# Performance work log

Measured on AMD Instinct MI355X. Metric: run time of the kernel, lower is better.

The kernel has to match this reference:

```python
import jax, jax.numpy as jnp
import numpy as np

B, S, D, H, HD, MLP = 2, 4096, 512, 8, 64, 2048
BLK, C = 128, 32  # Fixed1Pattern(block_size=128), Fixed2Pattern(block_size=128, c=32)
EPS = 1e-6


def _xavier(key, shape, fan_in, fan_out):
    lim = np.sqrt(6.0 / (fan_in + fan_out)).astype(np.float32)
    return jax.random.uniform(key, shape, jnp.float32, -lim, lim)


def setup_inputs() -> dict:
    key = jax.random.key(0)
    ks = jax.random.split(key, 9)
    return {
        "inputs": jax.random.normal(ks[0], (B, S, D), jnp.float32),
        "ln1_scale": jnp.ones((D,), jnp.float32),
        "ln1_bias": jnp.zeros((D,), jnp.float32),
        "wq": _xavier(ks[1], (D, H, HD), D, H * HD),
        "wk": _xavier(ks[2], (D, H, HD), D, H * HD),
        "wv": _xavier(ks[3], (D, H, HD), D, H * HD),
        "wo": _xavier(ks[4], (H, HD, D), H * HD, D),
        "ln2_scale": jnp.ones((D,), jnp.float32),
        "ln2_bias": jnp.zeros((D,), jnp.float32),
        "w1": _xavier(ks[5], (D, MLP), D, MLP),
        "b1": jax.random.normal(ks[6], (MLP,), jnp.float32) * 1e-6,
        "w2": _xavier(ks[7], (MLP, D), MLP, D),
        "b2": jax.random.normal(ks[8], (D,), jnp.float32) * 1e-6,
    }


def _layer_norm(x, scale, bias):
    mu = jnp.mean(x, axis=-1, keepdims=True)
    var = jnp.mean(jnp.square(x - mu), axis=-1, keepdims=True)
    return (x - mu) * jax.lax.rsqrt(var + EPS) * scale + bias


def _sparse_mask():
    # Union of causal Fixed1 (same block) and Fixed2 (last C columns of each block) patterns.
    i = jnp.arange(S)[:, None]
    j = jnp.arange(S)[None, :]
    causal = j <= i
    local = (i // BLK) == (j // BLK)            # Fixed1: within-block
    strided = (j % BLK) >= (BLK - C)            # Fixed2: block-summary columns
    return causal & (local | strided)           # [S, S] bool


def reference(inputs, ln1_scale, ln1_bias, wq, wk, wv, wo,
              ln2_scale, ln2_bias, w1, b1, w2, b2):
    x = _layer_norm(inputs, ln1_scale, ln1_bias)
    q = jnp.einsum("bsd,dhk->bshk", x, wq)
    k = jnp.einsum("bsd,dhk->bshk", x, wk)
    v = jnp.einsum("bsd,dhk->bshk", x, wv)
    scale = 1.0 / np.sqrt(HD).astype(np.float32)
    scores = jnp.einsum("bqhk,bshk->bhqs", q * scale, k)  # [B,H,S,S]
    mask = _sparse_mask()[None, None]
    scores = jnp.where(mask, scores, jnp.float32(-1e9))
    attn = jax.nn.softmax(scores, axis=-1)
    ctx = jnp.einsum("bhqs,bshk->bqhk", attn, v)
    attn_out = jnp.einsum("bqhk,hkd->bqd", ctx, wo)
    x = attn_out + inputs  # residual 1 (dropout deterministic)
    y = _layer_norm(x, ln2_scale, ln2_bias)
    y = jax.nn.gelu(y @ w1 + b1) @ w2 + b2  # MlpBlock
    return x + y
```

## Files before the change

kernel.cpp:

```cpp
#include <hip/hip_runtime.h>
#include <hip/hip_bf16.h>

typedef __attribute__((ext_vector_type(8))) __bf16 bf16x8;
typedef __attribute__((ext_vector_type(8))) short s16x8;
typedef __attribute__((ext_vector_type(4))) float f32x4;

#define NB 2
#define NS 4096
#define ND 512
#define NH 8
#define NHD 64
#define NMLP 2048

__device__ __forceinline__ unsigned short f2b(float f) {
  __hip_bfloat16 h = __float2bfloat16(f);
  return __builtin_bit_cast(unsigned short, h);
}

__device__ __forceinline__ float b2f(unsigned short u) {
  unsigned int x = (unsigned int)u << 16;
  return __builtin_bit_cast(float, x);
}

__device__ __forceinline__ float geluf(float x) {
  float u = 0.7978845608028654f * (x + 0.044715f * x * x * x);
  return x / (1.0f + __expf(-2.0f * u));
}

__device__ __forceinline__ float exp2_fast(float x) {
  float r;
  asm("v_exp_f32 %0, %1" : "=v"(r) : "v"(x));
  return r;
}

__device__ __forceinline__ void gload16(const void* g, void* l) {
  __builtin_amdgcn_global_load_lds((const __attribute__((address_space(1))) void*)g,
                                   (__attribute__((address_space(3))) void*)l, 16, 0, 0);
}

__global__ __launch_bounds__(256) void prep_ln(const float* __restrict__ wq,
                                               const float* __restrict__ wk,
                                               const float* __restrict__ wv,
                                               const float* __restrict__ wo,
                                               const float* __restrict__ w1,
                                               const float* __restrict__ w2,
                                               unsigned short* __restrict__ qkvT,
                                               unsigned short* __restrict__ woT,
                                               unsigned short* __restrict__ w1T,
                                               unsigned short* __restrict__ w2T,
                                               const float* __restrict__ x,
                                               const float* __restrict__ g,
                                               const float* __restrict__ bta,
                                               unsigned short* __restrict__ xout) {
  __shared__ unsigned short lt[64][66];
  const int t = threadIdx.x;
  if (blockIdx.x < 768) {
    const int tile = blockIdx.x;
    const float* src;
    unsigned short* dst;
    int R, C, tr, tc;
    float sc = 1.0f;
    if (tile < 256) {
      int seg = tile >> 6, tt = tile & 63;
      R = 512; C = 512;
      src = seg == 0 ? wq : seg == 1 ? wk : seg == 2 ? wv : wo;
      dst = (seg < 3) ? (qkvT + ((size_t)seg << 18)) : woT;
      if (seg == 0) sc = 0.18033688011112042f;
      tr = tt >> 3; tc = tt & 7;
    } else if (tile < 512) {
      int tt = tile - 256;
      R = 512; C = 2048; src = w1; dst = w1T;
      tr = tt >> 5; tc = tt & 31;
    } else {
      int tt = tile - 512;
      R = 2048; C = 512; src = w2; dst = w2T;
      tr = tt >> 3; tc = tt & 7;
    }
    const int r0 = tr * 64, c0 = tc * 64;
    const int fx = t & 15, fy = t >> 4;
#pragma unroll
    for (int p = 0; p < 4; ++p) {
      int rr = p * 16 + fy;
      float4 v = *(const float4*)&src[(size_t)(r0 + rr) * C + c0 + fx * 4];
      lt[rr][fx * 4 + 0] = f2b(v.x * sc);
      lt[rr][fx * 4 + 1] = f2b(v.y * sc);
      lt[rr][fx * 4 + 2] = f2b(v.z * sc);
      lt[rr][fx * 4 + 3] = f2b(v.w * sc);
    }
    __syncthreads();
#pragma unroll
    for (int p = 0; p < 4; ++p) {
      int cc = p * 16 + fy;
      ushort4 o;
      o.x = lt[fx * 4 + 0][cc];
      o.y = lt[fx * 4 + 1][cc];
      o.z = lt[fx * 4 + 2][cc];
      o.w = lt[fx * 4 + 3][cc];
      *(ushort4*)&dst[(size_t)(c0 + cc) * R + r0 + fx * 4] = o;
    }
  } else {
    const int l = t & 63, w = t >> 6;
    const size_t row = (size_t)(blockIdx.x - 768) * 4 + w;
    const float4* xr = (const float4*)(x + row * ND);
    float4 a = xr[l];
    float4 bq = xr[64 + l];
    float s = a.x + a.y + a.z + a.w + bq.x + bq.y + bq.z + bq.w;
    float ss = a.x * a.x + a.y * a.y + a.z * a.z + a.w * a.w +
               bq.x * bq.x + bq.y * bq.y + bq.z * bq.z + bq.w * bq.w;
#pragma unroll
    for (int msk = 1; msk <= 32; msk <<= 1) {
      s += __shfl_xor(s, msk);
      ss += __shfl_xor(ss, msk);
    }
    float mu = s * (1.0f / ND);
    float var = ss * (1.0f / ND) - mu * mu;
    float rr = rsqrtf(var + 1e-6f);
    const float4* g4 = (const float4*)g;
    const float4* b4 = (const float4*)bta;
    float4 g0 = g4[l], g1 = g4[64 + l], b0 = b4[l], b1 = b4[64 + l];
    ushort4 o0, o1;
    o0.x = f2b((a.x - mu) * rr * g0.x + b0.x);
    o0.y = f2b((a.y - mu) * rr * g0.y + b0.y);
    o0.z = f2b((a.z - mu) * rr * g0.z + b0.z);
    o0.w = f2b((a.w - mu) * rr * g0.w + b0.w);
    o1.x = f2b((bq.x - mu) * rr * g1.x + b1.x);
    o1.y = f2b((bq.y - mu) * rr * g1.y + b1.y);
    o1.z = f2b((bq.z - mu) * rr * g1.z + b1.z);
    o1.w = f2b((bq.w - mu) * rr * g1.w + b1.w);
    ushort4* orow = (ushort4*)(xout + row * ND);
    orow[l] = o0;
    orow[64 + l] = o1;
  }
}

__global__ __launch_bounds__(256) void ln_bf16_in(const unsigned short* __restrict__ x,
                                                  const float* __restrict__ g,
                                                  const float* __restrict__ bta,
                                                  unsigned short* __restrict__ out) {
  const int t = threadIdx.x, l = t & 63, w = t >> 6;
  const size_t row = (size_t)blockIdx.x * 4 + w;
  const s16x8 v = *(const s16x8*)&x[row * ND + l * 8];
  float xv[8];
  float s = 0.0f, ss = 0.0f;
#pragma unroll
  for (int i = 0; i < 8; ++i) {
    xv[i] = b2f((unsigned short)v[i]);
    s += xv[i];
    ss += xv[i] * xv[i];
  }
#pragma unroll
  for (int msk = 1; msk <= 32; msk <<= 1) {
    s += __shfl_xor(s, msk);
    ss += __shfl_xor(ss, msk);
  }
  float mu = s * (1.0f / ND);
  float var = ss * (1.0f / ND) - mu * mu;
  float rr = rsqrtf(var + 1e-6f);
  const float4* g4 = (const float4*)g;
  const float4* b4 = (const float4*)bta;
  float4 g0 = g4[2 * l], g1 = g4[2 * l + 1];
  float4 b0 = b4[2 * l], b1 = b4[2 * l + 1];
  s16x8 o;
  o[0] = (short)f2b((xv[0] - mu) * rr * g0.x + b0.x);
  o[1] = (short)f2b((xv[1] - mu) * rr * g0.y + b0.y);
  o[2] = (short)f2b((xv[2] - mu) * rr * g0.z + b0.z);
  o[3] = (short)f2b((xv[3] - mu) * rr * g0.w + b0.w);
  o[4] = (short)f2b((xv[4] - mu) * rr * g1.x + b1.x);
  o[5] = (short)f2b((xv[5] - mu) * rr * g1.y + b1.y);
  o[6] = (short)f2b((xv[6] - mu) * rr * g1.z + b1.z);
  o[7] = (short)f2b((xv[7] - mu) * rr * g1.w + b1.w);
  *(s16x8*)&out[row * ND + l * 8] = o;
}

template <int EPI>
__global__ __launch_bounds__(512) void gemm_bt(const unsigned short* __restrict__ A,
                                               const unsigned short* __restrict__ Bt,
                                               int M, int N, int K,
                                               unsigned short* __restrict__ ob,
                                               float* __restrict__ of,
                                               const float* __restrict__ addf,
                                               const float* __restrict__ bias) {
  __shared__ unsigned short lA[2][128 * 64];
  __shared__ unsigned short lB[2][128 * 64];
  const int t = threadIdx.x;
  const int l = t & 63, w = t >> 6;
  const int wr = w >> 2, wc = w & 3;
  const int gx = gridDim.x;
  const int nwg = gx * gridDim.y;
  const int fid = blockIdx.y * gx + blockIdx.x;
  const int q8 = nwg >> 3, r8 = nwg & 7, xcd = fid & 7, idx = fid >> 3;
  const int lid = (xcd < r8 ? xcd * (q8 + 1) : r8 * (q8 + 1) + (xcd - r8) * q8) + idx;
  const int bm = lid / gx, bn = lid % gx;
  const size_t rowBytes = (size_t)K * 2;
  const char* Ab = (const char*)A + (size_t)bm * 128 * rowBytes;
  const char* Bb = (const char*)Bt + (size_t)bn * 128 * rowBytes;
  const int sr0 = t >> 3;
  const int scb = (((t & 7) ^ ((t >> 3) & 7)) << 4);
  f32x4 acc[4][2] = {};

  auto stage = [&](int buf, int k0) {
    char* dA = (char*)&lA[buf][0] + t * 16;
    char* dB = (char*)&lB[buf][0] + t * 16;
#pragma unroll
    for (int i = 0; i < 2; ++i) {
      const size_t go = (size_t)(sr0 + i * 64) * rowBytes + 2 * k0 + scb;
      gload16(Ab + go, dA + i * 8192);
      gload16(Bb + go, dB + i * 8192);
    }
  };

  const int nkt = K >> 6;
  stage(0, 0);
  int cur = 0;
  for (int kt = 0; kt < nkt; ++kt) {
    if (kt + 1 < nkt) {
      stage(cur ^ 1, (kt + 1) * 64);
      asm volatile("s_waitcnt vmcnt(4)" ::: "memory");
    } else {
      asm volatile("s_waitcnt vmcnt(0)" ::: "memory");
    }
    __builtin_amdgcn_s_barrier();
    __builtin_amdgcn_sched_barrier(0);
#pragma unroll
    for (int ks = 0; ks < 2; ++ks) {
      const int xg = ((ks * 4 + (l >> 4)) ^ (l & 7)) * 8;
      bf16x8 aF[4], bF[2];
#pragma unroll
      for (int m = 0; m < 4; ++m)
        aF[m] = *(const bf16x8*)&lA[cur][(wr * 64 + m * 16 + (l & 15)) * 64 + xg];
#pragma unroll
      for (int n = 0; n < 2; ++n)
        bF[n] = *(const bf16x8*)&lB[cur][(wc * 32 + n * 16 + (l & 15)) * 64 + xg];
      __builtin_amdgcn_s_setprio(1);
#pragma unroll
      for (int m = 0; m < 4; ++m)
#pragma unroll
        for (int n = 0; n < 2; ++n)
          acc[m][n] = __builtin_amdgcn_mfma_f32_16x16x32_bf16(aF[m], bF[n], acc[m][n], 0, 0, 0);
      __builtin_amdgcn_s_setprio(0);
    }
    asm volatile("s_waitcnt lgkmcnt(0)" ::: "memory");
    __builtin_amdgcn_s_barrier();
    cur ^= 1;
  }
#pragma unroll
  for (int m = 0; m < 4; ++m)
#pragma unroll
    for (int n = 0; n < 2; ++n) {
      int row0 = bm * 128 + wr * 64 + m * 16 + (l >> 4) * 4;
      int col = bn * 128 + wc * 32 + n * 16 + (l & 15);
      if constexpr (EPI == 2) {
#pragma unroll
        for (int j = 0; j < 4; ++j) {
          size_t i = (size_t)(row0 + j) * NMLP + col;
          ob[i] = f2b(geluf(acc[m][n][j] + bias[col]));
        }
      } else {
#pragma unroll
        for (int j = 0; j < 4; ++j) {
          size_t i = (size_t)(row0 + j) * ND + col;
          of[i] = acc[m][n][j] + addf[i];
        }
      }
    }
}

template <int EPI>
__global__ __launch_bounds__(256) void gemm_bt64(const unsigned short* __restrict__ A,
                                                 const unsigned short* __restrict__ Bt,
                                                 int M, int N, int K,
                                                 unsigned short* __restrict__ ob,
                                                 float* __restrict__ of,
                                                 const float* __restrict__ addf,
                                                 const float* __restrict__ bias,
                                                 const unsigned short* __restrict__ addb) {
  __shared__ unsigned short lA[2][128 * 64];
  __shared__ unsigned short lB[2][64 * 64];
  const int t = threadIdx.x;
  const int l = t & 63, w = t >> 6;
  const int wr = w >> 1, wc = w & 1;
  const int gx = gridDim.x;
  const int nwg = gx * gridDim.y;
  const int fid = blockIdx.y * gx + blockIdx.x;
  const int q8 = nwg >> 3, r8 = nwg & 7, xcd = fid & 7, idx = fid >> 3;
  const int lid = (xcd < r8 ? xcd * (q8 + 1) : r8 * (q8 + 1) + (xcd - r8) * q8) + idx;
  const int bm = lid / gx, bn = lid % gx;
  const size_t rowBytes = (size_t)K * 2;
  const char* Ab = (const char*)A + (size_t)bm * 128 * rowBytes;
  const char* Bb = (const char*)Bt + (size_t)bn * 64 * rowBytes;
  const int sr0 = t >> 3;
  const int scb = (((t & 7) ^ ((t >> 3) & 7)) << 4);
  f32x4 acc[4][2] = {};

  auto stage = [&](int buf, int k0) {
    char* dA = (char*)&lA[buf][0] + t * 16;
#pragma unroll
    for (int i = 0; i < 4; ++i) {
      const size_t go = (size_t)(sr0 + i * 32) * rowBytes + 2 * k0 + scb;
      gload16(Ab + go, dA + i * 4096);
    }
    char* dB = (char*)&lB[buf][0] + t * 16;
#pragma unroll
    for (int i = 0; i < 2; ++i) {
      const size_t go = (size_t)(sr0 + i * 32) * rowBytes + 2 * k0 + scb;
      gload16(Bb + go, dB + i * 4096);
    }
  };

  const int nkt = K >> 6;
  stage(0, 0);
  int cur = 0;
  for (int kt = 0; kt < nkt; ++kt) {
    if (kt + 1 < nkt) {
      stage(cur ^ 1, (kt + 1) * 64);
      asm volatile("s_waitcnt vmcnt(6)" ::: "memory");
    } else {
      asm volatile("s_waitcnt vmcnt(0)" ::: "memory");
    }
    __builtin_amdgcn_s_barrier();
    __builtin_amdgcn_sched_barrier(0);
#pragma unroll
    for (int ks = 0; ks < 2; ++ks) {
      const int xg = ((ks * 4 + (l >> 4)) ^ (l & 7)) * 8;
      bf16x8 aF[4], bF[2];
#pragma unroll
      for (int m = 0; m < 4; ++m)
        aF[m] = *(const bf16x8*)&lA[cur][(wr * 64 + m * 16 + (l & 15)) * 64 + xg];
#pragma unroll
      for (int n = 0; n < 2; ++n)
        bF[n] = *(const bf16x8*)&lB[cur][(wc * 32 + n * 16 + (l & 15)) * 64 + xg];
      __builtin_amdgcn_s_setprio(1);
#pragma unroll
      for (int m = 0; m < 4; ++m)
#pragma unroll
        for (int n = 0; n < 2; ++n)
          acc[m][n] = __builtin_amdgcn_mfma_f32_16x16x32_bf16(aF[m], bF[n], acc[m][n], 0, 0, 0);
      __builtin_amdgcn_s_setprio(0);
    }
    asm volatile("s_waitcnt lgkmcnt(0)" ::: "memory");
    __builtin_amdgcn_s_barrier();
    cur ^= 1;
  }
#pragma unroll
  for (int m = 0; m < 4; ++m)
#pragma unroll
    for (int n = 0; n < 2; ++n) {
      int row0 = bm * 128 + wr * 64 + m * 16 + (l >> 4) * 4;
      int col = bn * 64 + wc * 32 + n * 16 + (l & 15);
      if constexpr (EPI == 0) {
        int part = col >> 9, nn = col & 511;
        int hh = nn >> 6, hd = nn & 63;
        int b = row0 >> 12, sidx0 = row0 & 4095;
        if (part < 2) {
#pragma unroll
          for (int j = 0; j < 4; ++j)
            ob[((((size_t)part * NB + b) * NH + hh) * NS + sidx0 + j) * NHD + hd] =
                f2b(acc[m][n][j]);
        } else {
          ushort4 o;
          o.x = f2b(acc[m][n][0]);
          o.y = f2b(acc[m][n][1]);
          o.z = f2b(acc[m][n][2]);
          o.w = f2b(acc[m][n][3]);
          *(ushort4*)&ob[(size_t)2 * NB * NH * NS * NHD +
                         (((size_t)b * NH + hh) * NHD + hd) * NS + sidx0] = o;
        }
      } else if constexpr (EPI == 1) {
#pragma unroll
        for (int j = 0; j < 4; ++j) {
          size_t i = (size_t)(row0 + j) * ND + col;
          ob[i] = f2b(acc[m][n][j] + addf[i]);
        }
      } else {
#pragma unroll
        for (int j = 0; j < 4; ++j) {
          size_t i = (size_t)(row0 + j) * ND + col;
          of[i] = acc[m][n][j] + bias[col] + b2f(addb[i]);
        }
      }
    }
}

__global__ __launch_bounds__(512, 4) void attn_sparse(const unsigned short* __restrict__ qm,
                                                      const unsigned short* __restrict__ km,
                                                      const unsigned short* __restrict__ vTg,
                                                      unsigned short* __restrict__ ctx) {
  __shared__ unsigned short kl[2][128 * 64];
  __shared__ unsigned short vt[2][64 * 128];
  __shared__ unsigned short pl[8][16 * 64];
  const int t = threadIdx.x, l = t & 63, w = t >> 6;
  const int bid = blockIdx.x;
  const int hh = bid & 7;
  const int jj = bid >> 3;
  const int b = jj >> 5;
  const int qb = (jj < 32) ? jj : 63 - jj;
  const size_t bh = ((size_t)b * NH + hh) * NS;
  const size_t bhd = ((size_t)b * NH + hh) * NHD;
  const int qrow0 = qb * 128 + w * 16;
  bf16x8 qa[2];
#pragma unroll
  for (int ks = 0; ks < 2; ++ks)
    qa[ks] = *(const bf16x8*)&qm[(bh + qrow0 + (l & 15)) * NHD + ks * 32 + (l >> 4) * 8];
  f32x4 c[4] = {};
  float mrun[4], lrun[4];
#pragma unroll
  for (int j = 0; j < 4; ++j) { mrun[j] = -1e30f; lrun[j] = 0.0f; }

  const int nsum128 = qb >> 2, rem = qb & 3;
  const int nSumCh = nsum128 + (rem ? 1 : 0);
  const int nch = nSumCh + 1;

  const int kr_ = t >> 3;
  const int ku_ = (t & 7) ^ (kr_ & 7);
  const int vr_ = t >> 4;
  const int vu_ = ((t & 15) & 8) | (((t & 15) & 7) ^ (vr_ & 7));

  auto keyOf = [&](int c2, int kk) -> int {
    return (c2 < nSumCh) ? ((c2 * 4 + (kk >> 5)) * 128 + 96 + (kk & 31)) : (qb * 128 + kk);
  };
  auto stage = [&](int buf, int c2) {
    const int krow0 = keyOf(c2, kr_);
    gload16(&km[(bh + krow0) * NHD + ku_ * 8], (char*)&kl[buf][0] + t * 16);
    const int krow1 = keyOf(c2, kr_ + 64);
    gload16(&km[(bh + krow1) * NHD + ku_ * 8], (char*)&kl[buf][0] + 8192 + t * 16);
    const int gk = keyOf(c2, vu_ * 8);
    gload16(&vTg[(bhd + vr_) * NS + gk], (char*)&vt[buf][0] + t * 16);
    gload16(&vTg[(bhd + vr_ + 32) * NS + gk], (char*)&vt[buf][0] + 8192 + t * 16);
  };

  const int e_ = l & 7, q_ = l >> 4;
  const int kx0 = (q_ ^ e_) * 8;
  const int kx1 = ((4 + q_) ^ e_) * 8;
  const int r4_ = (q_ & 1) << 2;

  stage(0, 0);
  int cur = 0;
  for (int ch = 0; ch < nch; ++ch) {
    if (ch + 1 < nch) {
      stage(cur ^ 1, ch + 1);
      asm volatile("s_waitcnt vmcnt(4)" ::: "memory");
    } else {
      asm volatile("s_waitcnt vmcnt(0)" ::: "memory");
    }
    __builtin_amdgcn_s_barrier();
    __builtin_amdgcn_sched_barrier(0);

    const bool isLocal = (ch == nch - 1);
    const bool isRem = (rem != 0) && !isLocal && (ch == nsum128);
    const int nT = isLocal ? (w + 1) : (isRem ? 2 * rem : 8);
    const int nTpl = isLocal ? ((w | 1) + 1) : nT;
    const int nKs = nTpl >> 1;

    f32x4 sf[8];
#pragma unroll
    for (int n = 0; n < 8; ++n) {
      if (n < nT) {
        const int row = n * 16 + (l & 15);
        const bf16x8 k0 = *(const bf16x8*)&kl[cur][row * 64 + kx0];
        const bf16x8 k1 = *(const bf16x8*)&kl[cur][row * 64 + kx1];
        f32x4 a = {};
        a = __builtin_amdgcn_mfma_f32_16x16x32_bf16(qa[0], k0, a, 0, 0, 0);
        a = __builtin_amdgcn_mfma_f32_16x16x32_bf16(qa[1], k1, a, 0, 0, 0);
        if (isLocal && n == w) {
#pragma unroll
          for (int j = 0; j < 4; ++j)
            if ((l & 15) > q_ * 4 + j) a[j] = -1e9f;
        }
        sf[n] = a;
      }
    }
    float cm[4];
#pragma unroll
    for (int j = 0; j < 4; ++j) cm[j] = -1e30f;
#pragma unroll
    for (int n = 0; n < 8; ++n)
      if (n < nT)
#pragma unroll
        for (int j = 0; j < 4; ++j) cm[j] = fmaxf(cm[j], sf[n][j]);
#pragma unroll
    for (int j = 0; j < 4; ++j) {
      cm[j] = fmaxf(cm[j], __shfl_xor(cm[j], 1));
      cm[j] = fmaxf(cm[j], __shfl_xor(cm[j], 2));
      cm[j] = fmaxf(cm[j], __shfl_xor(cm[j], 4));
      cm[j] = fmaxf(cm[j], __shfl_xor(cm[j], 8));
    }
    bool need = false;
#pragma unroll
    for (int j = 0; j < 4; ++j) need |= (cm[j] > mrun[j] + 11.5416f);
    if (__any(need)) {
      float al[4];
#pragma unroll
      for (int j = 0; j < 4; ++j) {
        float nm = fmaxf(mrun[j], cm[j]);
        al[j] = exp2_fast(mrun[j] - nm);
        mrun[j] = nm;
      }
#pragma unroll
      for (int n = 0; n < 4; ++n)
#pragma unroll
        for (int j = 0; j < 4; ++j) c[n][j] *= al[j];
#pragma unroll
      for (int j = 0; j < 4; ++j) lrun[j] *= al[j];
    }
    float rs[4] = {0.f, 0.f, 0.f, 0.f};
#pragma unroll
    for (int n = 0; n < 8; ++n)
      if (n < nT)
#pragma unroll
        for (int j = 0; j < 4; ++j) {
          float p = exp2_fast(sf[n][j] - mrun[j]);
          sf[n][j] = p;
          rs[j] += p;
        }
#pragma unroll
    for (int j = 0; j < 4; ++j) {
      rs[j] += __shfl_xor(rs[j], 1);
      rs[j] += __shfl_xor(rs[j], 2);
      rs[j] += __shfl_xor(rs[j], 4);
      rs[j] += __shfl_xor(rs[j], 8);
      lrun[j] += rs[j];
    }
#pragma unroll
    for (int h = 0; h < 2; ++h) {
      if (h * 4 < nTpl) {
#pragma unroll
        for (int n2 = 0; n2 < 4; ++n2) {
          const int n = h * 4 + n2;
          const int cu = n2 * 2 + ((l >> 3) & 1);
#pragma unroll
          for (int j = 0; j < 4; ++j) {
            if (n < nTpl) {
              unsigned short pv = 0;
              if (n < nT) pv = f2b(sf[n][j]);
              const int rowp = q_ * 4 + j;
              pl[w][rowp * 64 + (cu ^ (r4_ | j)) * 8 + e_] = pv;
            }
          }
        }
#pragma unroll
        for (int ks2 = 0; ks2 < 2; ++ks2) {
          const int ks = h * 2 + ks2;
          if (ks < nKs) {
            const bf16x8 pa =
                *(const bf16x8*)&pl[w][(l & 15) * 64 + (ks2 ? kx1 : kx0)];
#pragma unroll
            for (int nd = 0; nd < 4; ++nd) {
              const bf16x8 vb = *(const bf16x8*)&vt[cur][(nd * 16 + (l & 15)) * 128 +
                                                         ((ks & 2) << 5) +
                                                         (ks2 ? kx1 : kx0)];
              c[nd] = __builtin_amdgcn_mfma_f32_16x16x32_bf16(pa, vb, c[nd], 0, 0, 0);
            }
          }
        }
      }
    }
    __builtin_amdgcn_s_barrier();
    cur ^= 1;
  }
  float rinv[4];
#pragma unroll
  for (int j = 0; j < 4; ++j) rinv[j] = 1.0f / lrun[j];
#pragma unroll
  for (int n = 0; n < 4; ++n)
#pragma unroll
    for (int j = 0; j < 4; ++j) {
      int srow = qrow0 + q_ * 4 + j;
      int col = n * 16 + (l & 15);
      ctx[((size_t)b * NS + srow) * ND + hh * NHD + col] = f2b(c[n][j] * rinv[j]);
    }
}

extern "C" void kernel_launch(void* const* d_in, const int* in_sizes, int n_in,
                              void* d_out, int out_size, void* d_ws, size_t ws_size,
                              hipStream_t stream) {
  (void)in_sizes; (void)n_in; (void)out_size; (void)ws_size;
  const float* inputs = (const float*)d_in[0];
  const float* ln1s = (const float*)d_in[1];
  const float* ln1b = (const float*)d_in[2];
  const float* wq = (const float*)d_in[3];
  const float* wk = (const float*)d_in[4];
  const float* wv = (const float*)d_in[5];
  const float* wo = (const float*)d_in[6];
  const float* ln2s = (const float*)d_in[7];
  const float* ln2b = (const float*)d_in[8];
  const float* w1 = (const float*)d_in[9];
  const float* b1 = (const float*)d_in[10];
  const float* w2 = (const float*)d_in[11];
  const float* b2 = (const float*)d_in[12];
  float* out = (float*)d_out;

  unsigned short* xln = (unsigned short*)d_ws;
  unsigned short* xln2 = xln + (size_t)8192 * 512;
  unsigned short* ctx = xln2 + (size_t)8192 * 512;
  unsigned short* qkv = ctx + (size_t)8192 * 512;
  unsigned short* xresb = qkv + (size_t)3 * 8192 * 512;
  unsigned short* hbuf = xresb + (size_t)8192 * 512;
  unsigned short* qkvT = hbuf + (size_t)8192 * 2048;
  unsigned short* woT = qkvT + (size_t)1536 * 512;
  unsigned short* w1T = woT + (size_t)512 * 512;
  unsigned short* w2T = w1T + (size_t)2048 * 512;

  prep_ln<<<2816, 256, 0, stream>>>(wq, wk, wv, wo, w1, w2, qkvT, woT, w1T, w2T,
                                    inputs, ln1s, ln1b, xln);
  gemm_bt64<0><<<dim3(24, 64), 256, 0, stream>>>(xln, qkvT, 8192, 1536, 512,
                                                 qkv, nullptr, nullptr, nullptr, nullptr);
  attn_sparse<<<512, 512, 0, stream>>>(qkv, qkv + (size_t)8192 * 512,
                                       qkv + (size_t)2 * 8192 * 512, ctx);
  gemm_bt64<1><<<dim3(8, 64), 256, 0, stream>>>(ctx, woT, 8192, 512, 512,
                                                xresb, nullptr, inputs, nullptr, nullptr);
  ln_bf16_in<<<2048, 256, 0, stream>>>(xresb, ln2s, ln2b, xln2);
  gemm_bt<2><<<dim3(16, 64), 512, 0, stream>>>(xln2, w1T, 8192, 2048, 512,
                                               hbuf, nullptr, nullptr, b1);
  gemm_bt64<3><<<dim3(8, 64), 256, 0, stream>>>(hbuf, w2T, 8192, 512, 2048,
                                                nullptr, out, nullptr, b2, xresb);
}
```

Measured before the change: 145.1 us.

## Split sparse attention into single-wave blocks loading K/V directly from global

Restructures the sparse attention kernel from 512-thread blocks, where eight waves share double-buffered K/V tiles in LDS, to 4096 single-wave blocks. Each wave reads K and V fragments straight from global memory into MFMA operands. This removes the LDS staging, the barriers and the async pipelining, and spreads work across more blocks for better load balance. In exchange, the eight waves of a query block each re-read the same K/V data, relying on L2 or L1 hits, and the loads are no longer overlapped with compute through explicit prefetching.

After: 184.1 us. +26.9%, slower.

```diff
diff --git a/kernel.cpp b/kernel.cpp
--- a/kernel.cpp
+++ b/kernel.cpp
@@ -381,22 +381,23 @@
     }
 }
 
-__global__ __launch_bounds__(512, 4) void attn_sparse(const unsigned short* __restrict__ qm,
-                                                      const unsigned short* __restrict__ km,
-                                                      const unsigned short* __restrict__ vTg,
-                                                      unsigned short* __restrict__ ctx) {
-  __shared__ unsigned short kl[2][128 * 64];
-  __shared__ unsigned short vt[2][64 * 128];
-  __shared__ unsigned short pl[8][16 * 64];
-  const int t = threadIdx.x, l = t & 63, w = t >> 6;
+__global__ __launch_bounds__(64) void attn_sparse(const unsigned short* __restrict__ qm,
+                                                  const unsigned short* __restrict__ km,
+                                                  const unsigned short* __restrict__ vTg,
+                                                  unsigned short* __restrict__ ctx) {
+  __shared__ unsigned short pl[16 * 64];
+  const int l = threadIdx.x;
   const int bid = blockIdx.x;
   const int hh = bid & 7;
-  const int jj = bid >> 3;
-  const int b = jj >> 5;
-  const int qb = (jj < 32) ? jj : 63 - jj;
+  const int u_ = bid >> 3;
+  const int wp = u_ & 7;
+  const int v_ = u_ >> 3;
+  const int b = v_ >> 5;
+  const int k_ = v_ & 31;
+  const int qb = b ? (31 - k_) : k_;
   const size_t bh = ((size_t)b * NH + hh) * NS;
   const size_t bhd = ((size_t)b * NH + hh) * NHD;
-  const int qrow0 = qb * 128 + w * 16;
+  const int qrow0 = qb * 128 + wp * 16;
   bf16x8 qa[2];
 #pragma unroll
   for (int ks = 0; ks < 2; ++ks)
@@ -410,22 +411,8 @@
   const int nSumCh = nsum128 + (rem ? 1 : 0);
   const int nch = nSumCh + 1;
 
-  const int kr_ = t >> 3;
-  const int ku_ = (t & 7) ^ (kr_ & 7);
-  const int vr_ = t >> 4;
-  const int vu_ = ((t & 15) & 8) | (((t & 15) & 7) ^ (vr_ & 7));
-
   auto keyOf = [&](int c2, int kk) -> int {
     return (c2 < nSumCh) ? ((c2 * 4 + (kk >> 5)) * 128 + 96 + (kk & 31)) : (qb * 128 + kk);
-  };
-  auto stage = [&](int buf, int c2) {
-    const int krow0 = keyOf(c2, kr_);
-    gload16(&km[(bh + krow0) * NHD + ku_ * 8], (char*)&kl[buf][0] + t * 16);
-    const int krow1 = keyOf(c2, kr_ + 64);
-    gload16(&km[(bh + krow1) * NHD + ku_ * 8], (char*)&kl[buf][0] + 8192 + t * 16);
-    const int gk = keyOf(c2, vu_ * 8);
-    gload16(&vTg[(bhd + vr_) * NS + gk], (char*)&vt[buf][0] + t * 16);
-    gload16(&vTg[(bhd + vr_ + 32) * NS + gk], (char*)&vt[buf][0] + 8192 + t * 16);
   };
 
   const int e_ = l & 7, q_ = l >> 4;
@@ -433,22 +420,11 @@
   const int kx1 = ((4 + q_) ^ e_) * 8;
   const int r4_ = (q_ & 1) << 2;
 
-  stage(0, 0);
-  int cur = 0;
   for (int ch = 0; ch < nch; ++ch) {
-    if (ch + 1 < nch) {
-      stage(cur ^ 1, ch + 1);
-      asm volatile("s_waitcnt vmcnt(4)" ::: "memory");
-    } else {
-      asm volatile("s_waitcnt vmcnt(0)" ::: "memory");
-    }
-    __builtin_amdgcn_s_barrier();
-    __builtin_amdgcn_sched_barrier(0);
-
     const bool isLocal = (ch == nch - 1);
     const bool isRem = (rem != 0) && !isLocal && (ch == nsum128);
-    const int nT = isLocal ? (w + 1) : (isRem ? 2 * rem : 8);
-    const int nTpl = isLocal ? ((w | 1) + 1) : nT;
+    const int nT = isLocal ? (wp + 1) : (isRem ? 2 * rem : 8);
+    const int nTpl = isLocal ? ((wp | 1) + 1) : nT;
     const int nKs = nTpl >> 1;
 
     f32x4 sf[8];
@@ -456,12 +432,13 @@
     for (int n = 0; n < 8; ++n) {
       if (n < nT) {
         const int row = n * 16 + (l & 15);
-        const bf16x8 k0 = *(const bf16x8*)&kl[cur][row * 64 + kx0];
-        const bf16x8 k1 = *(const bf16x8*)&kl[cur][row * 64 + kx1];
+        const unsigned short* kp = &km[(bh + keyOf(ch, row)) * NHD];
+        const bf16x8 k0 = *(const bf16x8*)&kp[q_ * 8];
+        const bf16x8 k1 = *(const bf16x8*)&kp[32 + q_ * 8];
         f32x4 a = {};
         a = __builtin_amdgcn_mfma_f32_16x16x32_bf16(qa[0], k0, a, 0, 0, 0);
         a = __builtin_amdgcn_mfma_f32_16x16x32_bf16(qa[1], k1, a, 0, 0, 0);
-        if (isLocal && n == w) {
+        if (isLocal && n == wp) {
 #pragma unroll
           for (int j = 0; j < 4; ++j)
             if ((l & 15) > q_ * 4 + j) a[j] = -1e9f;
@@ -533,7 +510,7 @@
               unsigned short pv = 0;
               if (n < nT) pv = f2b(sf[n][j]);
               const int rowp = q_ * 4 + j;
-              pl[w][rowp * 64 + (cu ^ (r4_ | j)) * 8 + e_] = pv;
+              pl[rowp * 64 + (cu ^ (r4_ | j)) * 8 + e_] = pv;
             }
           }
         }
@@ -542,20 +519,18 @@
           const int ks = h * 2 + ks2;
           if (ks < nKs) {
             const bf16x8 pa =
-                *(const bf16x8*)&pl[w][(l & 15) * 64 + (ks2 ? kx1 : kx0)];
+                *(const bf16x8*)&pl[(l & 15) * 64 + (ks2 ? kx1 : kx0)];
+            const int gkv = keyOf(ch, ks * 32 + q_ * 8);
 #pragma unroll
             for (int nd = 0; nd < 4; ++nd) {
-              const bf16x8 vb = *(const bf16x8*)&vt[cur][(nd * 16 + (l & 15)) * 128 +
-                                                         ((ks & 2) << 5) +
-                                                         (ks2 ? kx1 : kx0)];
+              const bf16x8 vb =
+                  *(const bf16x8*)&vTg[(bhd + nd * 16 + (l & 15)) * NS + gkv];
               c[nd] = __builtin_amdgcn_mfma_f32_16x16x32_bf16(pa, vb, c[nd], 0, 0, 0);
             }
           }
         }
       }
     }
-    __builtin_amdgcn_s_barrier();
-    cur ^= 1;
   }
   float rinv[4];
 #pragma unroll
@@ -604,7 +579,7 @@
                                     inputs, ln1s, ln1b, xln);
   gemm_bt64<0><<<dim3(24, 64), 256, 0, stream>>>(xln, qkvT, 8192, 1536, 512,
                                                  qkv, nullptr, nullptr, nullptr, nullptr);
-  attn_sparse<<<512, 512, 0, stream>>>(qkv, qkv + (size_t)8192 * 512,
+  attn_sparse<<<4096, 64, 0, stream>>>(qkv, qkv + (size_t)8192 * 512,
                                        qkv + (size_t)2 * 8192 * 512, ctx);
   gemm_bt64<1><<<dim3(8, 64), 256, 0, stream>>>(ctx, woT, 8192, 512, 512,
                                                 xresb, nullptr, inputs, nullptr, nullptr);
```

## Split sparse attention key chunks across two blocks and add a merge kernel

Applied to the files above, without the earlier changes.

Each (batch, head, query-block) attention task is now split into two halves over its key chunks, with 1024 blocks each writing an unnormalized partial output plus running max and sum. A new merge kernel combines the two partials with log-sum-exp rescaling and writes the normalized context. The aim is to balance the triangular per-block workload and fill more CUs. The cost is an extra launch, extra global traffic for the partials (stored as bf16, with a small precision loss), and reuse of the MLP hidden buffer as scratch.

Measured after the change: 147.8 us. No clear change (+1.8%).

```diff
diff --git a/kernel.cpp b/kernel.cpp
--- a/kernel.cpp
+++ b/kernel.cpp
@@ -384,16 +384,20 @@
 __global__ __launch_bounds__(512, 4) void attn_sparse(const unsigned short* __restrict__ qm,
                                                       const unsigned short* __restrict__ km,
                                                       const unsigned short* __restrict__ vTg,
-                                                      unsigned short* __restrict__ ctx) {
+                                                      unsigned short* __restrict__ Op,
+                                                      float* __restrict__ mlp) {
   __shared__ unsigned short kl[2][128 * 64];
   __shared__ unsigned short vt[2][64 * 128];
   __shared__ unsigned short pl[8][16 * 64];
   const int t = threadIdx.x, l = t & 63, w = t >> 6;
   const int bid = blockIdx.x;
   const int hh = bid & 7;
-  const int jj = bid >> 3;
-  const int b = jj >> 5;
-  const int qb = (jj < 32) ? jj : 63 - jj;
+  const int u_ = bid >> 3;
+  const int half = u_ & 1;
+  const int j2 = u_ >> 1;
+  const int b = j2 >> 5;
+  const int k_ = j2 & 31;
+  const int qb = b ? (31 - k_) : k_;
   const size_t bh = ((size_t)b * NH + hh) * NS;
   const size_t bhd = ((size_t)b * NH + hh) * NHD;
   const int qrow0 = qb * 128 + w * 16;
@@ -409,6 +413,9 @@
   const int nsum128 = qb >> 2, rem = qb & 3;
   const int nSumCh = nsum128 + (rem ? 1 : 0);
   const int nch = nSumCh + 1;
+  const int h0 = (nSumCh + 1) >> 1;
+  const int chLo = half ? h0 : 0;
+  const int chHi = half ? nch : h0;
 
   const int kr_ = t >> 3;
   const int ku_ = (t & 7) ^ (kr_ & 7);
@@ -433,141 +440,185 @@
   const int kx1 = ((4 + q_) ^ e_) * 8;
   const int r4_ = (q_ & 1) << 2;
 
-  stage(0, 0);
-  int cur = 0;
-  for (int ch = 0; ch < nch; ++ch) {
-    if (ch + 1 < nch) {
-      stage(cur ^ 1, ch + 1);
-      asm volatile("s_waitcnt vmcnt(4)" ::: "memory");
-    } else {
-      asm volatile("s_waitcnt vmcnt(0)" ::: "memory");
-    }
-    __builtin_amdgcn_s_barrier();
-    __builtin_amdgcn_sched_barrier(0);
-
-    const bool isLocal = (ch == nch - 1);
-    const bool isRem = (rem != 0) && !isLocal && (ch == nsum128);
-    const int nT = isLocal ? (w + 1) : (isRem ? 2 * rem : 8);
-    const int nTpl = isLocal ? ((w | 1) + 1) : nT;
-    const int nKs = nTpl >> 1;
-
-    f32x4 sf[8];
-#pragma unroll
-    for (int n = 0; n < 8; ++n) {
-      if (n < nT) {
-        const int row = n * 16 + (l & 15);
-        const bf16x8 k0 = *(const bf16x8*)&kl[cur][row * 64 + kx0];
-        const bf16x8 k1 = *(const bf16x8*)&kl[cur][row * 64 + kx1];
-        f32x4 a = {};
-        a = __builtin_amdgcn_mfma_f32_16x16x32_bf16(qa[0], k0, a, 0, 0, 0);
-        a = __builtin_amdgcn_mfma_f32_16x16x32_bf16(qa[1], k1, a, 0, 0, 0);
-        if (isLocal && n == w) {
-#pragma unroll
-          for (int j = 0; j < 4; ++j)
-            if ((l & 15) > q_ * 4 + j) a[j] = -1e9f;
-        }
-        sf[n] = a;
-      }
-    }
-    float cm[4];
-#pragma unroll
-    for (int j = 0; j < 4; ++j) cm[j] = -1e30f;
-#pragma unroll
-    for (int n = 0; n < 8; ++n)
-      if (n < nT)
-#pragma unroll
-        for (int j = 0; j < 4; ++j) cm[j] = fmaxf(cm[j], sf[n][j]);
-#pragma unroll
-    for (int j = 0; j < 4; ++j) {
-      cm[j] = fmaxf(cm[j], __shfl_xor(cm[j], 1));
-      cm[j] = fmaxf(cm[j], __shfl_xor(cm[j], 2));
-      cm[j] = fmaxf(cm[j], __shfl_xor(cm[j], 4));
-      cm[j] = fmaxf(cm[j], __shfl_xor(cm[j], 8));
-    }
-    bool need = false;
-#pragma unroll
-    for (int j = 0; j < 4; ++j) need |= (cm[j] > mrun[j] + 11.5416f);
-    if (__any(need)) {
-      float al[4];
+  if (chLo < chHi) {
+    stage(0, chLo);
+    int cur = 0;
+    for (int ch = chLo; ch < chHi; ++ch) {
+      if (ch + 1 < chHi) {
+        stage(cur ^ 1, ch + 1);
+        asm volatile("s_waitcnt vmcnt(4)" ::: "memory");
+      } else {
+        asm volatile("s_waitcnt vmcnt(0)" ::: "memory");
+      }
+      __builtin_amdgcn_s_barrier();
+      __builtin_amdgcn_sched_barrier(0);
+
+      const bool isLocal = (ch == nch - 1);
+      const bool isRem = (rem != 0) && !isLocal && (ch == nsum128);
+      const int nT = isLocal ? (w + 1) : (isRem ? 2 * rem : 8);
+      const int nTpl = isLocal ? ((w | 1) + 1) : nT;
+      const int nKs = nTpl >> 1;
+
+      f32x4 sf[8];
+#pragma unroll
+      for (int n = 0; n < 8; ++n) {
+        if (n < nT) {
+          const int row = n * 16 + (l & 15);
+          const bf16x8 k0 = *(const bf16x8*)&kl[cur][row * 64 + kx0];
+          const bf16x8 k1 = *(const bf16x8*)&kl[cur][row * 64 + kx1];
+          f32x4 a = {};
+          a = __builtin_amdgcn_mfma_f32_16x16x32_bf16(qa[0], k0, a, 0, 0, 0);
+          a = __builtin_amdgcn_mfma_f32_16x16x32_bf16(qa[1], k1, a, 0, 0, 0);
+          if (isLocal && n == w) {
+#pragma unroll
+            for (int j = 0; j < 4; ++j)
+              if ((l & 15) > q_ * 4 + j) a[j] = -1e9f;
+          }
+          sf[n] = a;
+        }
+      }
+      float cm[4];
+#pragma unroll
+      for (int j = 0; j < 4; ++j) cm[j] = -1e30f;
+#pragma unroll
+      for (int n = 0; n < 8; ++n)
+        if (n < nT)
+#pragma unroll
+          for (int j = 0; j < 4; ++j) cm[j] = fmaxf(cm[j], sf[n][j]);
 #pragma unroll
       for (int j = 0; j < 4; ++j) {
-        float nm = fmaxf(mrun[j], cm[j]);
-        al[j] = exp2_fast(mrun[j] - nm);
-        mrun[j] = nm;
-      }
-#pragma unroll
-      for (int n = 0; n < 4; ++n)
-#pragma unroll
-        for (int j = 0; j < 4; ++j) c[n][j] *= al[j];
-#pragma unroll
-      for (int j = 0; j < 4; ++j) lrun[j] *= al[j];
-    }
-    float rs[4] = {0.f, 0.f, 0.f, 0.f};
-#pragma unroll
-    for (int n = 0; n < 8; ++n)
-      if (n < nT)
+        cm[j] = fmaxf(cm[j], __shfl_xor(cm[j], 1));
+        cm[j] = fmaxf(cm[j], __shfl_xor(cm[j], 2));
+        cm[j] = fmaxf(cm[j], __shfl_xor(cm[j], 4));
+        cm[j] = fmaxf(cm[j], __shfl_xor(cm[j], 8));
+      }
+      bool need = false;
+#pragma unroll
+      for (int j = 0; j < 4; ++j) need |= (cm[j] > mrun[j] + 11.5416f);
+      if (__any(need)) {
+        float al[4];
 #pragma unroll
         for (int j = 0; j < 4; ++j) {
-          float p = exp2_fast(sf[n][j] - mrun[j]);
-          sf[n][j] = p;
-          rs[j] += p;
-        }
-#pragma unroll
-    for (int j = 0; j < 4; ++j) {
-      rs[j] += __shfl_xor(rs[j], 1);
-      rs[j] += __shfl_xor(rs[j], 2);
-      rs[j] += __shfl_xor(rs[j], 4);
-      rs[j] += __shfl_xor(rs[j], 8);
-      lrun[j] += rs[j];
-    }
-#pragma unroll
-    for (int h = 0; h < 2; ++h) {
-      if (h * 4 < nTpl) {
-#pragma unroll
-        for (int n2 = 0; n2 < 4; ++n2) {
-          const int n = h * 4 + n2;
-          const int cu = n2 * 2 + ((l >> 3) & 1);
+          float nm = fmaxf(mrun[j], cm[j]);
+          al[j] = exp2_fast(mrun[j] - nm);
+          mrun[j] = nm;
+        }
+#pragma unroll
+        for (int n = 0; n < 4; ++n)
+#pragma unroll
+          for (int j = 0; j < 4; ++j) c[n][j] *= al[j];
+#pragma unroll
+        for (int j = 0; j < 4; ++j) lrun[j] *= al[j];
+      }
+      float rs[4] = {0.f, 0.f, 0.f, 0.f};
+#pragma unroll
+      for (int n = 0; n < 8; ++n)
+        if (n < nT)
 #pragma unroll
           for (int j = 0; j < 4; ++j) {
-            if (n < nTpl) {
-              unsigned short pv = 0;
-              if (n < nT) pv = f2b(sf[n][j]);
-              const int rowp = q_ * 4 + j;
-              pl[w][rowp * 64 + (cu ^ (r4_ | j)) * 8 + e_] = pv;
+            float p = exp2_fast(sf[n][j] - mrun[j]);
+            sf[n][j] = p;
+            rs[j] += p;
+          }
+#pragma unroll
+      for (int j = 0; j < 4; ++j) {
+        rs[j] += __shfl_xor(rs[j], 1);
+        rs[j] += __shfl_xor(rs[j], 2);
+        rs[j] += __shfl_xor(rs[j], 4);
+        rs[j] += __shfl_xor(rs[j], 8);
+        lrun[j] += rs[j];
+      }
+#pragma unroll
+      for (int h = 0; h < 2; ++h) {
+        if (h * 4 < nTpl) {
+#pragma unroll
+          for (int n2 = 0; n2 < 4; ++n2) {
+            const int n = h * 4 + n2;
+            const int cu = n2 * 2 + ((l >> 3) & 1);
+#pragma unroll
+            for (int j = 0; j < 4; ++j) {
+              if (n < nTpl) {
+                unsigned short pv = 0;
+                if (n < nT) pv = f2b(sf[n][j]);
+                const int rowp = q_ * 4 + j;
+                pl[w][rowp * 64 + (cu ^ (r4_ | j)) * 8 + e_] = pv;
+              }
             }
           }
-        }
-#pragma unroll
-        for (int ks2 = 0; ks2 < 2; ++ks2) {
-          const int ks = h * 2 + ks2;
-          if (ks < nKs) {
-            const bf16x8 pa =
-                *(const bf16x8*)&pl[w][(l & 15) * 64 + (ks2 ? kx1 : kx0)];
-#pragma unroll
-            for (int nd = 0; nd < 4; ++nd) {
-              const bf16x8 vb = *(const bf16x8*)&vt[cur][(nd * 16 + (l & 15)) * 128 +
-                                                         ((ks & 2) << 5) +
-                                                         (ks2 ? kx1 : kx0)];
-              c[nd] = __builtin_amdgcn_mfma_f32_16x16x32_bf16(pa, vb, c[nd], 0, 0, 0);
+#pragma unroll
+          for (int ks2 = 0; ks2 < 2; ++ks2) {
+            const int ks = h * 2 + ks2;
+            if (ks < nKs) {
+              const bf16x8 pa =
+                  *(const bf16x8*)&pl[w][(l & 15) * 64 + (ks2 ? kx1 : kx0)];
+#pragma unroll
+              for (int nd = 0; nd < 4; ++nd) {
+                const bf16x8 vb = *(const bf16x8*)&vt[cur][(nd * 16 + (l & 15)) * 128 +
+                                                           ((ks & 2) << 5) +
+                                                           (ks2 ? kx1 : kx0)];
+                c[nd] = __builtin_amdgcn_mfma_f32_16x16x32_bf16(pa, vb, c[nd], 0, 0, 0);
+              }
             }
           }
         }
       }
-    }
-    __builtin_amdgcn_s_barrier();
-    cur ^= 1;
-  }
-  float rinv[4];
-#pragma unroll
-  for (int j = 0; j < 4; ++j) rinv[j] = 1.0f / lrun[j];
+      __builtin_amdgcn_s_barrier();
+      cur ^= 1;
+    }
+  }
+  const size_t pbase = (size_t)bid * (128 * 64);
 #pragma unroll
   for (int n = 0; n < 4; ++n)
 #pragma unroll
     for (int j = 0; j < 4; ++j) {
-      int srow = qrow0 + q_ * 4 + j;
-      int col = n * 16 + (l & 15);
-      ctx[((size_t)b * NS + srow) * ND + hh * NHD + col] = f2b(c[n][j] * rinv[j]);
-    }
+      const int prow = w * 16 + q_ * 4 + j;
+      Op[pbase + prow * 64 + n * 16 + (l & 15)] = f2b(c[n][j]);
+    }
+  if ((l & 15) == 0) {
+#pragma unroll
+    for (int j = 0; j < 4; ++j) {
+      const size_t mlb = ((size_t)bid * 128 + w * 16 + q_ * 4 + j) * 2;
+      mlp[mlb] = mrun[j];
+      mlp[mlb + 1] = lrun[j];
+    }
+  }
+}
+
+__global__ __launch_bounds__(256) void attn_merge(const unsigned short* __restrict__ Op,
+                                                  const float* __restrict__ mlp,
+                                                  unsigned short* __restrict__ ctx) {
+  const int bid = blockIdx.x;
+  const int hh = bid & 7;
+  const int j2 = bid >> 3;
+  const int b = j2 >> 5;
+  const int k_ = j2 & 31;
+  const int qb = b ? (31 - k_) : k_;
+  const int t = threadIdx.x;
+  const int row = t >> 1;
+  const int c0 = (t & 1) * 32;
+  const int sidS = (j2 * 2 + 0) * 8 + hh;
+  const int sidT = (j2 * 2 + 1) * 8 + hh;
+  const size_t mb1 = ((size_t)sidS * 128 + row) * 2;
+  const size_t mb2 = ((size_t)sidT * 128 + row) * 2;
+  const float m1 = mlp[mb1], l1 = mlp[mb1 + 1];
+  const float m2 = mlp[mb2], l2 = mlp[mb2 + 1];
+  const float m = fmaxf(m1, m2);
+  const float a1 = exp2_fast(m1 - m), a2 = exp2_fast(m2 - m);
+  const float rinv = 1.0f / (a1 * l1 + a2 * l2);
+  const unsigned short* p1 = &Op[((size_t)sidS * 128 + row) * 64 + c0];
+  const unsigned short* p2 = &Op[((size_t)sidT * 128 + row) * 64 + c0];
+  unsigned short* po = &ctx[((size_t)b * NS + qb * 128 + row) * ND + hh * NHD + c0];
+#pragma unroll
+  for (int i = 0; i < 32; i += 8) {
+    const s16x8 v1 = *(const s16x8*)(p1 + i);
+    const s16x8 v2 = *(const s16x8*)(p2 + i);
+    s16x8 o;
+#pragma unroll
+    for (int jj = 0; jj < 8; ++jj)
+      o[jj] = (short)f2b((a1 * b2f((unsigned short)v1[jj]) +
+                          a2 * b2f((unsigned short)v2[jj])) * rinv);
+    *(s16x8*)(po + i) = o;
+  }
 }
 
 extern "C" void kernel_launch(void* const* d_in, const int* in_sizes, int n_in,
@@ -600,12 +651,16 @@
   unsigned short* w1T = woT + (size_t)512 * 512;
   unsigned short* w2T = w1T + (size_t)2048 * 512;
 
+  unsigned short* Op = hbuf;
+  float* mlbuf = (float*)(hbuf + (size_t)1024 * 128 * 64);
+
   prep_ln<<<2816, 256, 0, stream>>>(wq, wk, wv, wo, w1, w2, qkvT, woT, w1T, w2T,
                                     inputs, ln1s, ln1b, xln);
   gemm_bt64<0><<<dim3(24, 64), 256, 0, stream>>>(xln, qkvT, 8192, 1536, 512,
                                                  qkv, nullptr, nullptr, nullptr, nullptr);
-  attn_sparse<<<512, 512, 0, stream>>>(qkv, qkv + (size_t)8192 * 512,
-                                       qkv + (size_t)2 * 8192 * 512, ctx);
+  attn_sparse<<<1024, 512, 0, stream>>>(qkv, qkv + (size_t)8192 * 512,
+                                        qkv + (size_t)2 * 8192 * 512, Op, mlbuf);
+  attn_merge<<<512, 256, 0, stream>>>(Op, mlbuf, ctx);
   gemm_bt64<1><<<dim3(8, 64), 256, 0, stream>>>(ctx, woT, 8192, 512, 512,
                                                 xresb, nullptr, inputs, nullptr, nullptr);
   ln_bf16_in<<<2048, 256, 0, stream>>>(xresb, ln2s, ln2b, xln2);
```
